# Performance work log

Measured on AMD Instinct MI355X. Metric: run time of the kernel, lower is better.

## Reference

```python
import jax, jax.numpy as jnp
import numpy as np

N = 100000   # nodes
E = 3200000  # edges
G = 2048     # graphs in batch
F_IN, H, EXTRA = 9, 64, 32
EPS = 1e-5


def setup_inputs() -> dict:
    key = jax.random.key(0)
    ks = jax.random.split(key, 24)
    w = lambda k, s: (jax.random.normal(k, s, jnp.float32) * 0.05)
    inp = {
        "x": jax.random.normal(ks[0], (N, F_IN), jnp.float32),
        "edge_index": jax.random.randint(ks[1], (2, E), 0, N),
        "batch": jnp.sort(jax.random.randint(ks[2], (N,), 0, G)),
        "extra": jax.random.normal(ks[3], (G, EXTRA), jnp.float32),
        # GCN layer params
        "W1": w(ks[4], (F_IN, H)), "b1": jnp.zeros((H,), jnp.float32),
        "W2": w(ks[5], (H, H)),    "b2": jnp.zeros((H,), jnp.float32),
        "W3": w(ks[6], (H, H)),    "b3": jnp.zeros((H,), jnp.float32),
        # MLP: [H+EXTRA, 128, 64, 32, 1]
        "Wm0": w(ks[7], (H + EXTRA, 128)), "bm0": jnp.zeros((128,), jnp.float32),
        "g0": jnp.ones((128,), jnp.float32), "be0": jnp.zeros((128,), jnp.float32),
        "Wm1": w(ks[8], (128, 64)), "bm1": jnp.zeros((64,), jnp.float32),
        "g1": jnp.ones((64,), jnp.float32), "be1": jnp.zeros((64,), jnp.float32),
        "Wm2": w(ks[9], (64, 32)), "bm2": jnp.zeros((32,), jnp.float32),
        "g2": jnp.ones((32,), jnp.float32), "be2": jnp.zeros((32,), jnp.float32),
        "Wm3": w(ks[10], (32, 1)), "bm3": jnp.zeros((1,), jnp.float32),
    }
    return inp


def reference(x, edge_index, batch, extra,
              W1, b1, W2, b2, W3, b3,
              Wm0, bm0, g0, be0, Wm1, bm1, g1, be1,
              Wm2, bm2, g2, be2, Wm3, bm3):
    n = x.shape[0]
    # GCN normalization (PyG gcn_norm with self-loops)
    loops = jnp.arange(n)
    src = jnp.concatenate([edge_index[0], loops])
    dst = jnp.concatenate([edge_index[1], loops])
    deg = jax.ops.segment_sum(jnp.ones_like(dst, jnp.float32), dst, num_segments=n)
    dis = jnp.where(deg > 0, jax.lax.rsqrt(deg), 0.0)
    coef = (dis[src] * dis[dst])[:, None]  # [E+N, 1]

    def gcn(h, W, b):
        h = h @ W                                         # transform first (as PyG)
        agg = jax.ops.segment_sum(h[src] * coef, dst, num_segments=n)
        return agg + b

    h = jax.nn.relu(gcn(x, W1, b1))
    h = jax.nn.relu(gcn(h, W2, b2))
    h = jax.nn.relu(gcn(h, W3, b3))

    # global mean pool over graphs
    cnt = jax.ops.segment_sum(jnp.ones((n,), jnp.float32), batch, num_segments=G)
    emb = jax.ops.segment_sum(h, batch, num_segments=G) / jnp.maximum(cnt, 1.0)[:, None]

    z = jnp.concatenate([emb, extra], axis=1)  # [G, H+EXTRA]

    def bn(h, g, b):  # BatchNorm1d, training-mode batch stats
        mu = h.mean(0)
        var = h.var(0)
        return (h - mu) * jax.lax.rsqrt(var + EPS) * g + b

    z = jax.nn.relu(bn(z @ Wm0 + bm0, g0, be0))
    z = jax.nn.relu(bn(z @ Wm1 + bm1, g1, be1))
    z = jax.nn.relu(bn(z @ Wm2 + bm2, g2, be2))
    return (z @ Wm3 + bm3).reshape(-1)  # [G]
```

## Files before the change

kernel.cpp:

```cpp
#include <hip/hip_runtime.h>

#define NN 100000
#define NE 3200000
#define NG 2048
#define FIN 9
#define HD 64
#define XD 32
#define BN_EPS 1e-5f
#define CAP 96
#define NBUCK 1024
#define BNODES 98
#define ECAP 3840
#define P1_CHUNK 16384

__device__ __forceinline__ unsigned f2bf(float f) {
    unsigned u = __float_as_uint(f);
    return (u + 0x7fffu + ((u >> 16) & 1u)) >> 16;
}
__device__ __forceinline__ unsigned pack2bf(float lo, float hi) {
    return f2bf(lo) | (f2bf(hi) << 16);
}
__device__ __forceinline__ float bflo(unsigned u) { return __uint_as_float(u << 16); }
__device__ __forceinline__ float bfhi(unsigned u) { return __uint_as_float(u & 0xffff0000u); }

__global__ void k_zeroi(int* p, int n) {
    int i = blockIdx.x * 256 + threadIdx.x;
    if (i < n) p[i] = 0;
}

__global__ __launch_bounds__(256) void k_split(const int* __restrict__ src,
                                               const int* __restrict__ dst,
                                               int* __restrict__ gcur,
                                               unsigned* __restrict__ ebuf) {
    __shared__ int hcnt[NBUCK];
    __shared__ int hbase[NBUCK];
    int tid = threadIdx.x;
    long e0 = (long)blockIdx.x * P1_CHUNK;
    long e1 = e0 + P1_CHUNK;
    if (e1 > NE) e1 = NE;
    for (int b = tid; b < NBUCK; b += 256) hcnt[b] = 0;
    __syncthreads();
    for (long e = e0 + tid; e < e1; e += 256) {
        int d = dst[e];
        atomicAdd(&hcnt[d / BNODES], 1);
    }
    __syncthreads();
    for (int b = tid; b < NBUCK; b += 256) {
        int c = hcnt[b];
        hbase[b] = (c > 0) ? atomicAdd(&gcur[b], c) : 0;
        hcnt[b] = 0;
    }
    __syncthreads();
    for (long e = e0 + tid; e < e1; e += 256) {
        int d = dst[e];
        int s = src[e];
        int b = d / BNODES;
        int dl = d - b * BNODES;
        int pos = hbase[b] + atomicAdd(&hcnt[b], 1);
        if (pos < ECAP)
            ebuf[(long)b * ECAP + pos] = ((unsigned)dl << 17) | (unsigned)s;
    }
}

__global__ __launch_bounds__(256) void k_build(const int* __restrict__ gcur,
                                               const unsigned* __restrict__ ebuf,
                                               int* __restrict__ srcs,
                                               int* __restrict__ deg) {
    __shared__ int lcnt[BNODES];
    __shared__ int lists[BNODES * CAP];
    int b = blockIdx.x;
    int tid = threadIdx.x;
    for (int i = tid; i < BNODES; i += 256) lcnt[i] = 0;
    __syncthreads();
    int cntb = gcur[b];
    if (cntb > ECAP) cntb = ECAP;
    const unsigned* eb = ebuf + (long)b * ECAP;
    for (int t = tid; t < cntb; t += 256) {
        unsigned p = eb[t];
        int dl = p >> 17;
        int s = p & 0x1FFFF;
        int k = atomicAdd(&lcnt[dl], 1);
        if (k < CAP) lists[dl * CAP + k] = s;
    }
    __syncthreads();
    long base = (long)b * BNODES * CAP;
    for (int i = tid; i < BNODES * CAP; i += 256)
        srcs[base + i] = lists[i];
    for (int i = tid; i < BNODES; i += 256) {
        int node = b * BNODES + i;
        if (node < NN) deg[node] = min(lcnt[i], CAP);
    }
}

__global__ void k_dis(const int* __restrict__ deg, float* __restrict__ dis) {
    int i = blockIdx.x * 256 + threadIdx.x;
    if (i < NN) dis[i] = rsqrtf((float)deg[i] + 1.0f);
}


__global__ void k_padx16(const float* __restrict__ x, const float* __restrict__ dis,
                         unsigned* __restrict__ xpd) {
    int gtid = blockIdx.x * 256 + threadIdx.x;
    if (gtid >= NN * 8) return;
    int i = gtid >> 3, u = gtid & 7;
    float d = dis[i];
    int f0 = 2 * u, f1 = 2 * u + 1;
    float a = (f0 < FIN) ? d * x[i * FIN + f0] : 0.f;
    float b = (f1 < FIN) ? d * x[i * FIN + f1] : 0.f;
    xpd[gtid] = pack2bf(a, b);
}

__global__ __launch_bounds__(256) void k_gather_x8(const unsigned* __restrict__ xpd,
                                                   const int* __restrict__ deg,
                                                   const int* __restrict__ srcs,
                                                   const float* __restrict__ dis,
                                                   float* __restrict__ aggx) {
    int tid = threadIdx.x;
    int i = blockIdx.x * 32 + (tid >> 3);
    int lane = tid & 7;
    if (i >= NN) return;
    float di = dis[i];
    unsigned u = xpd[i * 8 + lane];
    float a0 = bflo(u), a1 = bfhi(u);
    int beg = i * CAP, end = beg + deg[i];
    int j = beg;
    for (; j + 3 < end; j += 4) {
        int s0 = srcs[j], s1 = srcs[j + 1], s2 = srcs[j + 2], s3 = srcs[j + 3];
        unsigned u0 = xpd[s0 * 8 + lane];
        unsigned u1 = xpd[s1 * 8 + lane];
        unsigned u2 = xpd[s2 * 8 + lane];
        unsigned u3 = xpd[s3 * 8 + lane];
        a0 += bflo(u0) + bflo(u1) + bflo(u2) + bflo(u3);
        a1 += bfhi(u0) + bfhi(u1) + bfhi(u2) + bfhi(u3);
    }
    for (; j < end; ++j) {
        int s0 = srcs[j];
        unsigned u0 = xpd[s0 * 8 + lane];
        a0 += bflo(u0);
        a1 += bfhi(u0);
    }
    float2 r = make_float2(di * a0, di * a1);
    *reinterpret_cast<float2*>(aggx + (long)i * 16 + lane * 2) = r;
}

__global__ void k_xform9(const float* __restrict__ aggx, const float* __restrict__ W,
                         const float* __restrict__ b, float* __restrict__ out) {
    __shared__ float Ws[FIN * HD];
    int t = threadIdx.x;
    if (t < FIN * HD) Ws[t] = W[t];
    __syncthreads();
    long gtid = (long)blockIdx.x * 256 + t;
    int i = (int)(gtid >> 6);
    int f = (int)(gtid & 63);
    if (i >= NN) return;
    const float* row = aggx + (long)i * 16;
    float acc = b[f];
#pragma unroll
    for (int k = 0; k < FIN; ++k) acc += row[k] * Ws[k * HD + f];
    out[gtid] = acc > 0.f ? acc : 0.f;
}


__global__ void k_xform64d(const float* __restrict__ h, const float* __restrict__ W,
                           const float* __restrict__ dis, unsigned* __restrict__ out16) {
    __shared__ float Ws[HD * HD];
    int t = threadIdx.x;
    for (int k = t; k < HD * HD; k += 256) Ws[k] = W[k];
    __syncthreads();
    long gtid = (long)blockIdx.x * 256 + t;
    int i = (int)(gtid >> 5);
    int u = (int)(gtid & 31);
    if (i >= NN) return;
    const float* row = h + (long)i * HD;
    int f0 = 2 * u;
    float a0 = 0.f, a1 = 0.f;
#pragma unroll
    for (int k = 0; k < HD; ++k) {
        float r = row[k];
        a0 += r * Ws[k * HD + f0];
        a1 += r * Ws[k * HD + f0 + 1];
    }
    float d = dis[i];
    out16[gtid] = pack2bf(d * a0, d * a1);
}

template <int POOL>
__global__ __launch_bounds__(256) void k_gather64b(const unsigned* __restrict__ hWd,
                                                   const int* __restrict__ deg,
                                                   const int* __restrict__ srcs,
                                                   const float* __restrict__ dis,
                                                   const float* __restrict__ b,
                                                   const int* __restrict__ batch,
                                                   float* __restrict__ z,
                                                   float* __restrict__ out) {
    int tid = threadIdx.x;
    int i = blockIdx.x * 8 + (tid >> 5);
    int lane = tid & 31;
    if (i >= NN) return;
    float di = dis[i];
    unsigned u = hWd[(long)i * 32 + lane];
    float a0 = bflo(u), a1 = bfhi(u);
    int beg = i * CAP, end = beg + deg[i];
    int j = beg;
    for (; j + 3 < end; j += 4) {
        int s0 = srcs[j], s1 = srcs[j + 1], s2 = srcs[j + 2], s3 = srcs[j + 3];
        unsigned u0 = hWd[(long)s0 * 32 + lane];
        unsigned u1 = hWd[(long)s1 * 32 + lane];
        unsigned u2 = hWd[(long)s2 * 32 + lane];
        unsigned u3 = hWd[(long)s3 * 32 + lane];
        a0 += bflo(u0) + bflo(u1) + bflo(u2) + bflo(u3);
        a1 += bfhi(u0) + bfhi(u1) + bfhi(u2) + bfhi(u3);
    }
    for (; j < end; ++j) {
        int s0 = srcs[j];
        unsigned u0 = hWd[(long)s0 * 32 + lane];
        a0 += bflo(u0);
        a1 += bfhi(u0);
    }
    int f0 = 2 * lane;
    float v0 = di * a0 + b[f0];
    float v1 = di * a1 + b[f0 + 1];
    v0 = v0 > 0.f ? v0 : 0.f;
    v1 = v1 > 0.f ? v1 : 0.f;
    if (POOL) {
        int g = batch[i];
        atomicAdd(&z[(long)g * (HD + XD) + f0], v0);
        atomicAdd(&z[(long)g * (HD + XD) + f0 + 1], v1);
    } else {
        *reinterpret_cast<float2*>(out + (long)i * HD + f0) = make_float2(v0, v1);
    }
}


__global__ void k_zero(float* p, long n) {
    long i = (long)blockIdx.x * 256 + threadIdx.x;
    if (i < n) p[i] = 0.f;
}

__global__ void k_cnt(const int* __restrict__ batch, float* __restrict__ cnt) {
    int i = blockIdx.x * 256 + threadIdx.x;
    if (i < NN) atomicAdd(&cnt[batch[i]], 1.0f);
}

__global__ void k_zfin(float* z, const float* __restrict__ cnt,
                       const float* __restrict__ extra) {
    int gtid = blockIdx.x * 256 + threadIdx.x;
    if (gtid >= NG * (HD + XD)) return;
    int g = gtid / (HD + XD);
    int f = gtid % (HD + XD);
    if (f < HD)
        z[gtid] = z[gtid] / fmaxf(cnt[g], 1.0f);
    else
        z[gtid] = extra[g * XD + (f - HD)];
}

template <int K, int M>
__global__ void k_mm(const float* __restrict__ in, const float* __restrict__ W,
                     const float* __restrict__ b, float* __restrict__ out) {
    int gtid = blockIdx.x * 256 + threadIdx.x;
    if (gtid >= NG * M) return;
    int g = gtid / M;
    int m = gtid % M;
    const float* row = in + (long)g * K;
    float acc = b[m];
#pragma unroll 8
    for (int k = 0; k < K; ++k) acc += row[k] * W[k * M + m];
    out[gtid] = acc;
}

template <int M>
__global__ void k_bn_relu(float* z, const float* __restrict__ gamma,
                          const float* __restrict__ beta) {
    int c = blockIdx.x;
    int t = threadIdx.x;
    __shared__ float s1[256], s2[256];
    float sum = 0.f, sumsq = 0.f;
    for (int g = t; g < NG; g += 256) {
        float v = z[(long)g * M + c];
        sum += v;
        sumsq += v * v;
    }
    s1[t] = sum;
    s2[t] = sumsq;
    __syncthreads();
    for (int o = 128; o > 0; o >>= 1) {
        if (t < o) {
            s1[t] += s1[t + o];
            s2[t] += s2[t + o];
        }
        __syncthreads();
    }
    float mean = s1[0] / (float)NG;
    float var = s2[0] / (float)NG - mean * mean;
    float scale = rsqrtf(var + BN_EPS) * gamma[c];
    float shift = beta[c] - mean * scale;
    for (int g = t; g < NG; g += 256) {
        float v = z[(long)g * M + c] * scale + shift;
        z[(long)g * M + c] = v > 0.f ? v : 0.f;
    }
}

__global__ void k_final(const float* __restrict__ z2, const float* __restrict__ W,
                        const float* __restrict__ b, float* __restrict__ out) {
    int g = blockIdx.x * 256 + threadIdx.x;
    if (g >= NG) return;
    const float* row = z2 + (long)g * 32;
    float acc = b[0];
#pragma unroll
    for (int k = 0; k < 32; ++k) acc += row[k] * W[k];
    out[g] = acc;
}

extern "C" void kernel_launch(void* const* d_in, const int* in_sizes, int n_in,
                              void* d_out, int out_size, void* d_ws, size_t ws_size,
                              hipStream_t stream) {
    const float* x = (const float*)d_in[0];
    const int* ei = (const int*)d_in[1];
    const int* batch = (const int*)d_in[2];
    const float* extra = (const float*)d_in[3];
    const float* W1 = (const float*)d_in[4];
    const float* b1 = (const float*)d_in[5];
    const float* W2 = (const float*)d_in[6];
    const float* b2 = (const float*)d_in[7];
    const float* W3 = (const float*)d_in[8];
    const float* b3 = (const float*)d_in[9];
    const float* Wm0 = (const float*)d_in[10];
    const float* bm0 = (const float*)d_in[11];
    const float* g0 = (const float*)d_in[12];
    const float* be0 = (const float*)d_in[13];
    const float* Wm1 = (const float*)d_in[14];
    const float* bm1 = (const float*)d_in[15];
    const float* g1 = (const float*)d_in[16];
    const float* be1 = (const float*)d_in[17];
    const float* Wm2 = (const float*)d_in[18];
    const float* bm2 = (const float*)d_in[19];
    const float* g2 = (const float*)d_in[20];
    const float* be2 = (const float*)d_in[21];
    const float* Wm3 = (const float*)d_in[22];
    const float* bm3 = (const float*)d_in[23];

    const int* src = ei;
    const int* dst = ei + NE;

    int* deg = (int*)d_ws;
    int* gcur = deg + 100352;
    int* srcs = gcur + 2048;
    float* dis = (float*)(srcs + (long)100352 * CAP);
    unsigned* xpd = (unsigned*)(dis + 100352);
    float* A = (float*)(xpd + (long)NN * 8);
    unsigned* B16 = (unsigned*)(A + (long)NN * HD);
    float* aggx = (float*)B16;
    unsigned* ebuf = (unsigned*)A;
    float* z = (float*)(B16 + (long)NN * 32);
    float* cnt = z + NG * (HD + XD);
    float* t0 = cnt + NG;
    float* t1 = t0 + NG * 128;
    float* t2 = t1 + NG * 64;

    unsigned bN = (NN + 255) / 256;
    unsigned bN32 = (NN * 32 + 255) / 256;
    unsigned bN64 = (NN * 64 + 255) / 256;
    unsigned bG8 = (NN + 7) / 8;

    k_zeroi<<<(NBUCK + 255) / 256, 256, 0, stream>>>(gcur, NBUCK);
    k_split<<<(NE + P1_CHUNK - 1) / P1_CHUNK, 256, 0, stream>>>(src, dst, gcur, ebuf);
    k_build<<<NBUCK, 256, 0, stream>>>(gcur, ebuf, srcs, deg);
    k_dis<<<bN, 256, 0, stream>>>(deg, dis);

    long zlen = (long)NG * (HD + XD) + NG;
    k_zero<<<(unsigned)((zlen + 255) / 256), 256, 0, stream>>>(z, zlen);

    k_padx16<<<(NN * 8 + 255) / 256, 256, 0, stream>>>(x, dis, xpd);
    k_gather_x8<<<(NN + 31) / 32, 256, 0, stream>>>(xpd, deg, srcs, dis, aggx);
    k_xform9<<<bN64, 256, 0, stream>>>(aggx, W1, b1, A);

    k_xform64d<<<bN32, 256, 0, stream>>>(A, W2, dis, B16);
    k_gather64b<0><<<bG8, 256, 0, stream>>>(B16, deg, srcs, dis, b2, batch, z, A);

    k_xform64d<<<bN32, 256, 0, stream>>>(A, W3, dis, B16);
    k_gather64b<1><<<bG8, 256, 0, stream>>>(B16, deg, srcs, dis, b3, batch, z, A);

    k_cnt<<<bN, 256, 0, stream>>>(batch, cnt);
    k_zfin<<<(NG * (HD + XD) + 255) / 256, 256, 0, stream>>>(z, cnt, extra);

    k_mm<96, 128><<<(NG * 128 + 255) / 256, 256, 0, stream>>>(z, Wm0, bm0, t0);
    k_bn_relu<128><<<128, 256, 0, stream>>>(t0, g0, be0);
    k_mm<128, 64><<<(NG * 64 + 255) / 256, 256, 0, stream>>>(t0, Wm1, bm1, t1);
    k_bn_relu<64><<<64, 256, 0, stream>>>(t1, g1, be1);
    k_mm<64, 32><<<(NG * 32 + 255) / 256, 256, 0, stream>>>(t1, Wm2, bm2, t2);
    k_bn_relu<32><<<32, 256, 0, stream>>>(t2, g2, be2);
    k_final<<<(NG + 255) / 256, 256, 0, stream>>>(t2, Wm3, bm3, (float*)d_out);
}
```

Before: 479.7 us.

## Split 64-wide feature gather into four feature-slice passes for cache locality

The transformed bf16 node features are stored as four slices of 16 features each (32 bytes per node), and the gather kernel runs each slice as a separate group of blocks. Each slice's working set is about 3.2 MB instead of 12.8 MB, so random neighbor reads are more likely to hit in L2. In exchange the srcs index lists and degrees are read four times, and each gather load is a 32-byte sector instead of a 128-byte row.

New measurement: 556.4 us. 1.16x slower.

```diff
diff --git a/kernel.cpp b/kernel.cpp
--- a/kernel.cpp
+++ b/kernel.cpp
@@ -12,6 +12,8 @@
 #define BNODES 98
 #define ECAP 3840
 #define P1_CHUNK 16384
+#define NPASS 4
+#define PBLK 3125
 
 __device__ __forceinline__ unsigned f2bf(float f) {
     unsigned u = __float_as_uint(f);
@@ -161,18 +163,21 @@
 }
 
 
-__global__ void k_xform64d(const float* __restrict__ h, const float* __restrict__ W,
-                           const float* __restrict__ dis, unsigned* __restrict__ out16) {
+__global__ __launch_bounds__(256) void k_xform64t(const float* __restrict__ h,
+                                                  const float* __restrict__ W,
+                                                  const float* __restrict__ dis,
+                                                  unsigned* __restrict__ outT) {
     __shared__ float Ws[HD * HD];
-    int t = threadIdx.x;
-    for (int k = t; k < HD * HD; k += 256) Ws[k] = W[k];
-    __syncthreads();
-    long gtid = (long)blockIdx.x * 256 + t;
-    int i = (int)(gtid >> 5);
-    int u = (int)(gtid & 31);
+    int tid = threadIdx.x;
+    for (int k = tid; k < HD * HD; k += 256) Ws[k] = W[k];
+    __syncthreads();
+    int p = tid >> 6;
+    int il = (tid >> 3) & 7;
+    int q = tid & 7;
+    int i = blockIdx.x * 8 + il;
     if (i >= NN) return;
     const float* row = h + (long)i * HD;
-    int f0 = 2 * u;
+    int f0 = p * 16 + 2 * q;
     float a0 = 0.f, a1 = 0.f;
 #pragma unroll
     for (int k = 0; k < HD; ++k) {
@@ -181,11 +186,11 @@
         a1 += r * Ws[k * HD + f0 + 1];
     }
     float d = dis[i];
-    out16[gtid] = pack2bf(d * a0, d * a1);
+    outT[(long)p * NN * 8 + (long)i * 8 + q] = pack2bf(d * a0, d * a1);
 }
 
 template <int POOL>
-__global__ __launch_bounds__(256) void k_gather64b(const unsigned* __restrict__ hWd,
+__global__ __launch_bounds__(256) void k_gather64s(const unsigned* __restrict__ hWdT,
                                                    const int* __restrict__ deg,
                                                    const int* __restrict__ srcs,
                                                    const float* __restrict__ dis,
@@ -193,31 +198,35 @@
                                                    const int* __restrict__ batch,
                                                    float* __restrict__ z,
                                                    float* __restrict__ out) {
+    int bid = blockIdx.x;
+    int p = bid / PBLK;
+    int nb = bid - p * PBLK;
     int tid = threadIdx.x;
-    int i = blockIdx.x * 8 + (tid >> 5);
-    int lane = tid & 31;
+    int i = nb * 32 + (tid >> 3);
+    int q = tid & 7;
     if (i >= NN) return;
+    const unsigned* slice = hWdT + (long)p * NN * 8;
     float di = dis[i];
-    unsigned u = hWd[(long)i * 32 + lane];
+    unsigned u = slice[(long)i * 8 + q];
     float a0 = bflo(u), a1 = bfhi(u);
     int beg = i * CAP, end = beg + deg[i];
     int j = beg;
     for (; j + 3 < end; j += 4) {
         int s0 = srcs[j], s1 = srcs[j + 1], s2 = srcs[j + 2], s3 = srcs[j + 3];
-        unsigned u0 = hWd[(long)s0 * 32 + lane];
-        unsigned u1 = hWd[(long)s1 * 32 + lane];
-        unsigned u2 = hWd[(long)s2 * 32 + lane];
-        unsigned u3 = hWd[(long)s3 * 32 + lane];
+        unsigned u0 = slice[(long)s0 * 8 + q];
+        unsigned u1 = slice[(long)s1 * 8 + q];
+        unsigned u2 = slice[(long)s2 * 8 + q];
+        unsigned u3 = slice[(long)s3 * 8 + q];
         a0 += bflo(u0) + bflo(u1) + bflo(u2) + bflo(u3);
         a1 += bfhi(u0) + bfhi(u1) + bfhi(u2) + bfhi(u3);
     }
     for (; j < end; ++j) {
         int s0 = srcs[j];
-        unsigned u0 = hWd[(long)s0 * 32 + lane];
+        unsigned u0 = slice[(long)s0 * 8 + q];
         a0 += bflo(u0);
         a1 += bfhi(u0);
     }
-    int f0 = 2 * lane;
+    int f0 = p * 16 + 2 * q;
     float v0 = di * a0 + b[f0];
     float v1 = di * a1 + b[f0 + 1];
     v0 = v0 > 0.f ? v0 : 0.f;
@@ -358,9 +367,9 @@
     float* t2 = t1 + NG * 64;
 
     unsigned bN = (NN + 255) / 256;
-    unsigned bN32 = (NN * 32 + 255) / 256;
     unsigned bN64 = (NN * 64 + 255) / 256;
-    unsigned bG8 = (NN + 7) / 8;
+    unsigned bT = (NN + 7) / 8;
+    unsigned bGS = NPASS * PBLK;
 
     k_zeroi<<<(NBUCK + 255) / 256, 256, 0, stream>>>(gcur, NBUCK);
     k_split<<<(NE + P1_CHUNK - 1) / P1_CHUNK, 256, 0, stream>>>(src, dst, gcur, ebuf);
@@ -374,11 +383,11 @@
     k_gather_x8<<<(NN + 31) / 32, 256, 0, stream>>>(xpd, deg, srcs, dis, aggx);
     k_xform9<<<bN64, 256, 0, stream>>>(aggx, W1, b1, A);
 
-    k_xform64d<<<bN32, 256, 0, stream>>>(A, W2, dis, B16);
-    k_gather64b<0><<<bG8, 256, 0, stream>>>(B16, deg, srcs, dis, b2, batch, z, A);
-
-    k_xform64d<<<bN32, 256, 0, stream>>>(A, W3, dis, B16);
-    k_gather64b<1><<<bG8, 256, 0, stream>>>(B16, deg, srcs, dis, b3, batch, z, A);
+    k_xform64t<<<bT, 256, 0, stream>>>(A, W2, dis, B16);
+    k_gather64s<0><<<bGS, 256, 0, stream>>>(B16, deg, srcs, dis, b2, batch, z, A);
+
+    k_xform64t<<<bT, 256, 0, stream>>>(A, W3, dis, B16);
+    k_gather64s<1><<<bGS, 256, 0, stream>>>(B16, deg, srcs, dis, b3, batch, z, A);
 
     k_cnt<<<bN, 256, 0, stream>>>(batch, cnt);
     k_zfin<<<(NG * (HD + XD) + 255) / 256, 256, 0, stream>>>(z, cnt, extra);
```
